# Optimization experiments

Measured on AMD Instinct MI355X. Metric: run time of the kernel, lower is better.

Reference implementation:

```python
import jax, jax.numpy as jnp
import numpy as np

NUM_HEADS = 16


def setup_inputs() -> dict:
    key = jax.random.key(0)
    ks = jax.random.split(key, 5)
    B, S, D = 2, 2048, 1024
    scale = 1.0 / np.sqrt(D)
    return {
        "hidden_states": jax.random.normal(ks[0], (B, S, D), dtype=jnp.float32),
        "Wq": jax.random.normal(ks[1], (D, D), dtype=jnp.float32) * scale,
        "bq": jnp.zeros((D,), jnp.float32),
        "Wk": jax.random.normal(ks[2], (D, D), dtype=jnp.float32) * scale,
        "bk": jnp.zeros((D,), jnp.float32),
        "Wv": jax.random.normal(ks[3], (D, D), dtype=jnp.float32) * scale,
        "bv": jnp.zeros((D,), jnp.float32),
        "Wo": jax.random.normal(ks[4], (D, D), dtype=jnp.float32) * scale,
        "bo": jnp.zeros((D,), jnp.float32),
    }


def reference(hidden_states, Wq, bq, Wk, bk, Wv, bv, Wo, bo):
    B, S, D = hidden_states.shape
    H = NUM_HEADS
    Dh = D // H

    def split_heads(x):  # [B,S,D] -> [B,H,S,Dh]
        return x.reshape(B, S, H, Dh).transpose(0, 2, 1, 3)

    q = split_heads(hidden_states @ Wq + bq)
    k = split_heads(hidden_states @ Wk + bk)
    v = split_heads(hidden_states @ Wv + bv)

    # causal additive mask: -inf strictly above the diagonal (triu, diagonal=1)
    i = jnp.arange(S)
    causal = jnp.where(i[None, :] > i[:, None], -jnp.inf, 0.0).astype(hidden_states.dtype)  # [S,S]

    scores = jnp.einsum("bhsd,bhtd->bhst", q, k) / jnp.sqrt(jnp.asarray(Dh, hidden_states.dtype))
    scores = scores + causal[None, None, :, :]
    weights = jax.nn.softmax(scores, axis=-1)  # [B,H,S,S]
    ctx = jnp.einsum("bhst,bhtd->bhsd", weights, v)
    ctx = ctx.transpose(0, 2, 1, 3).reshape(B, S, D)
    return ctx @ Wo + bo
```

## Files before the change

kernel.cpp:

```cpp
#include <hip/hip_runtime.h>
#include <math.h>

#define SEQ    2048
#define DMODEL 1024
#define NHEADS 16
#define DHEAD  64
#define NBATCH 2

typedef __attribute__((ext_vector_type(8)))  short bf16x8;
typedef __attribute__((ext_vector_type(4)))  float f32x4;
typedef __attribute__((ext_vector_type(16))) float f32x16;

__device__ __forceinline__ unsigned short f2bf(float f) {
    union { float f; unsigned u; } v; v.f = f;
    unsigned r = (v.u + 0x7FFF + ((v.u >> 16) & 1)) >> 16;
    return (unsigned short)r;
}

__device__ __forceinline__ unsigned cvt_pk_bf16(float lo, float hi) {
    unsigned r;
    asm("v_cvt_pk_bf16_f32 %0, %1, %2" : "=v"(r) : "v"(lo), "v"(hi));
    return r;
}

__device__ __forceinline__ void gload16(const void* g, void* l) {
    __builtin_amdgcn_global_load_lds(
        (const __attribute__((address_space(1))) unsigned*)g,
        (__attribute__((address_space(3))) unsigned*)l, 16, 0, 0);
}

__global__ __launch_bounds__(256)
void cast_bf16_kernel(const float* __restrict__ in, unsigned short* __restrict__ out) {
    const size_t g8 = ((size_t)blockIdx.x * 256 + threadIdx.x) * 8;
    float4 a = *reinterpret_cast<const float4*>(in + g8);
    float4 b = *reinterpret_cast<const float4*>(in + g8 + 4);
    bf16x8 o;
    o[0] = (short)f2bf(a.x); o[1] = (short)f2bf(a.y);
    o[2] = (short)f2bf(a.z); o[3] = (short)f2bf(a.w);
    o[4] = (short)f2bf(b.x); o[5] = (short)f2bf(b.y);
    o[6] = (short)f2bf(b.z); o[7] = (short)f2bf(b.w);
    *reinterpret_cast<bf16x8*>(out + g8) = o;
}

__global__ __launch_bounds__(256)
void wt_cast4_kernel(const float* __restrict__ W0, const float* __restrict__ W1,
                     const float* __restrict__ W2, const float* __restrict__ W3,
                     unsigned short* __restrict__ out) {
    __shared__ float tile[64][65];
    const int wsel = blockIdx.y;
    const float* W = (wsel == 0) ? W0 : (wsel == 1) ? W1 : (wsel == 2) ? W2 : W3;
    unsigned short* Wt = out + (size_t)wsel * 1024 * 1024;

    const int nt  = blockIdx.x & 15;
    const int kt  = blockIdx.x >> 4;
    const int tid = threadIdx.x;

#pragma unroll
    for (int r = 0; r < 4; ++r) {
        int kl = r * 16 + (tid >> 4);
        int nl = (tid & 15) * 4;
        float4 v = *reinterpret_cast<const float4*>(
            &W[(size_t)(kt * 64 + kl) * 1024 + nt * 64 + nl]);
        tile[kl][nl + 0] = v.x; tile[kl][nl + 1] = v.y;
        tile[kl][nl + 2] = v.z; tile[kl][nl + 3] = v.w;
    }
    __syncthreads();

    const int n  = tid >> 2;
    const int kc = (tid & 3) * 16;
    bf16x8 o0, o1;
#pragma unroll
    for (int i = 0; i < 8; ++i) o0[i] = (short)f2bf(tile[kc + i][n]);
#pragma unroll
    for (int i = 0; i < 8; ++i) o1[i] = (short)f2bf(tile[kc + 8 + i][n]);
    unsigned short* op = Wt + (size_t)(nt * 64 + n) * 1024 + kt * 64 + kc;
    *reinterpret_cast<bf16x8*>(op)     = o0;
    *reinterpret_cast<bf16x8*>(op + 8) = o1;
}

template <int MODE>
__global__ __launch_bounds__(256)
void gemm_bf16(const unsigned short* __restrict__ A,
               const unsigned short* __restrict__ Bt,
               const float* __restrict__ bias0, const float* __restrict__ bias1,
               const float* __restrict__ bias2,
               float* __restrict__ Cf,
               unsigned short* __restrict__ Qo, unsigned short* __restrict__ Ko,
               unsigned short* __restrict__ Vo,
               int M, int N, int K) {
    __shared__ unsigned short As[2][128 * 32];
    __shared__ unsigned short Bs[2][128 * 32];

    const int tid  = threadIdx.x;
    const int bm   = blockIdx.y * 128;
    const int bn   = blockIdx.x * 128;
    const int w    = tid >> 6;
    const int lane = tid & 63;
    const int lrow = lane & 15;
    const int lk   = lane >> 4;
    const int wm0  = (w >> 1) * 64;
    const int wn0  = (w & 1) * 64;

    const int boff0 = tid * 16;
    const int boff1 = 4096 + tid * 16;
    const int row0  = tid >> 2;
    const int row1  = 64 + row0;
    const int c     = tid & 3;
    const int sw0   = (c ^ ((row0 >> 1) & 3)) * 8;
    const int sw1   = (c ^ ((row1 >> 1) & 3)) * 8;

    const unsigned short* Ag = A  + (size_t)bm * K;
    const unsigned short* Bg = Bt + (size_t)bn * K;

    f32x4 acc[4][4];
#pragma unroll
    for (int i = 0; i < 4; ++i)
#pragma unroll
        for (int j = 0; j < 4; ++j) acc[i][j] = (f32x4){0.f, 0.f, 0.f, 0.f};

    const int NT = K / 32;
    {
        gload16(Ag + (size_t)row0 * K + sw0, (char*)&As[0][0] + boff0);
        gload16(Ag + (size_t)row1 * K + sw1, (char*)&As[0][0] + boff1);
        gload16(Bg + (size_t)row0 * K + sw0, (char*)&Bs[0][0] + boff0);
        gload16(Bg + (size_t)row1 * K + sw1, (char*)&Bs[0][0] + boff1);
    }
    __syncthreads();

    int buf = 0;
    for (int kt = 0; kt < NT; ++kt) {
        if (kt + 1 < NT) {
            const int k0 = (kt + 1) * 32;
            gload16(Ag + (size_t)row0 * K + k0 + sw0, (char*)&As[buf ^ 1][0] + boff0);
            gload16(Ag + (size_t)row1 * K + k0 + sw1, (char*)&As[buf ^ 1][0] + boff1);
            gload16(Bg + (size_t)row0 * K + k0 + sw0, (char*)&Bs[buf ^ 1][0] + boff0);
            gload16(Bg + (size_t)row1 * K + k0 + sw1, (char*)&Bs[buf ^ 1][0] + boff1);
        }

        bf16x8 af[4], bf[4];
#pragma unroll
        for (int mg = 0; mg < 4; ++mg) {
            const int r = wm0 + mg * 16 + lrow;
            af[mg] = *reinterpret_cast<const bf16x8*>(
                (char*)&As[buf][0] + r * 64 + ((lk ^ ((r >> 1) & 3)) * 16));
        }
#pragma unroll
        for (int ng = 0; ng < 4; ++ng) {
            const int r = wn0 + ng * 16 + lrow;
            bf[ng] = *reinterpret_cast<const bf16x8*>(
                (char*)&Bs[buf][0] + r * 64 + ((lk ^ ((r >> 1) & 3)) * 16));
        }
#pragma unroll
        for (int mg = 0; mg < 4; ++mg)
#pragma unroll
            for (int ng = 0; ng < 4; ++ng)
                acc[mg][ng] = __builtin_amdgcn_mfma_f32_16x16x32_bf16(
                    af[mg], bf[ng], acc[mg][ng], 0, 0, 0);

        __syncthreads();
        buf ^= 1;
    }

    if (MODE == 0) {
        const int type = bn >> 10;
        const int nloc = bn & 1023;
        const float* bias = (type == 0) ? bias0 : (type == 1) ? bias1 : bias2;
        const float QSCALE = 0.125f * 1.44269504088896f;
#pragma unroll
        for (int ng = 0; ng < 4; ++ng) {
            const int col = nloc + wn0 + ng * 16 + lrow;
            const float bv = bias[col];
            const int h = col >> 6, d = col & 63;
#pragma unroll
            for (int mg = 0; mg < 4; ++mg) {
#pragma unroll
                for (int j = 0; j < 4; ++j) {
                    const int row = bm + wm0 + mg * 16 + lk * 4 + j;
                    const int b = row >> 11, s = row & 2047;
                    const float val = acc[mg][ng][j] + bv;
                    if (type == 0)
                        Qo[((size_t)(b * 16 + h) * SEQ + s) * 64 + d] = f2bf(val * QSCALE);
                    else if (type == 1)
                        Ko[((size_t)(b * 16 + h) * SEQ + s) * 64 + d] = f2bf(val);
                    else
                        Vo[((size_t)(b * 16 + h) * 64 + d) * SEQ + s] = f2bf(val);
                }
            }
        }
    } else {
#pragma unroll
        for (int ng = 0; ng < 4; ++ng) {
            const int col = bn + wn0 + ng * 16 + lrow;
            const float bv = bias0[col];
#pragma unroll
            for (int mg = 0; mg < 4; ++mg) {
#pragma unroll
                for (int j = 0; j < 4; ++j) {
                    const int row = bm + wm0 + mg * 16 + lk * 4 + j;
                    Cf[(size_t)row * N + col] = acc[mg][ng][j] + bv;
                }
            }
        }
    }
}

__global__ __launch_bounds__(256)
void attn_mfma_kernel(const unsigned short* __restrict__ Qg,
                      const unsigned short* __restrict__ Kg,
                      const unsigned short* __restrict__ Vtg,
                      unsigned short* __restrict__ CTX) {
    __shared__ __align__(16) unsigned short Ks[2][64 * 64];
    __shared__ __align__(16) unsigned short Vt[2][64 * 64];

    const int bid = blockIdx.x;
    const int xcd = bid & 7;
    const int s   = bid >> 3;
    const int bh  = xcd * 4 + (s & 3);
    const int rb  = s >> 2;
    const int b  = bh >> 4;
    const int h  = bh & 15;
    const int r0 = rb * 128;
    const int tid  = threadIdx.x;
    const int w    = tid >> 6;
    const int lane = tid & 63;
    const int qcol = lane & 31;
    const int hlf  = lane >> 5;
    const int wr0  = r0 + w * 32;
    const int qrow = wr0 + qcol;

    const unsigned short* Kb = Kg + ((size_t)bh * SEQ) * DHEAD;
    const unsigned short* Vb = Vtg + ((size_t)bh * DHEAD) * SEQ;

    bf16x8 qf[4];
    {
        const unsigned short* qp = Qg + ((size_t)bh * SEQ + qrow) * DHEAD + hlf * 8;
#pragma unroll
        for (int ksub = 0; ksub < 4; ++ksub)
            qf[ksub] = *reinterpret_cast<const bf16x8*>(qp + ksub * 16);
    }

    f32x16 O0, O1;
#pragma unroll
    for (int r = 0; r < 16; ++r) { O0[r] = 0.f; O1[r] = 0.f; }
    float m = -1e30f, l = 0.f;

    const int srow = tid >> 2;
    const int c0   = (tid & 3) * 16;
    const int sb0  = srow * 128 + ((c0 * 2) ^ ((srow & 7) << 4));
    const int sb1  = srow * 128 + (((c0 + 8) * 2) ^ ((srow & 7) << 4));

    bf16x8 rk0, rk1, rv0, rv1;
    {
        const unsigned short* kp = Kb + (size_t)srow * DHEAD + c0;
        const unsigned short* vp = Vb + (size_t)srow * SEQ + c0;
        rk0 = *reinterpret_cast<const bf16x8*>(kp);
        rk1 = *reinterpret_cast<const bf16x8*>(kp + 8);
        rv0 = *reinterpret_cast<const bf16x8*>(vp);
        rv1 = *reinterpret_cast<const bf16x8*>(vp + 8);
    }

    const int ntile = (r0 + 128) / 64;
    for (int t = 0; t < ntile; ++t) {
        const int j0 = t * 64;
        const int buf = t & 1;
        *reinterpret_cast<bf16x8*>((char*)&Ks[buf][0] + sb0) = rk0;
        *reinterpret_cast<bf16x8*>((char*)&Ks[buf][0] + sb1) = rk1;
        *reinterpret_cast<bf16x8*>((char*)&Vt[buf][0] + sb0) = rv0;
        *reinterpret_cast<bf16x8*>((char*)&Vt[buf][0] + sb1) = rv1;
        __syncthreads();
        if (t + 1 < ntile) {
            const int j1 = j0 + 64;
            const unsigned short* kp = Kb + (size_t)(j1 + srow) * DHEAD + c0;
            const unsigned short* vp = Vb + (size_t)srow * SEQ + j1 + c0;
            rk0 = *reinterpret_cast<const bf16x8*>(kp);
            rk1 = *reinterpret_cast<const bf16x8*>(kp + 8);
            rv0 = *reinterpret_cast<const bf16x8*>(vp);
            rv1 = *reinterpret_cast<const bf16x8*>(vp + 8);
        }

        if (j0 <= wr0 + 31) {
            f32x16 S[2];
#pragma unroll
            for (int r = 0; r < 16; ++r) { S[0][r] = 0.f; S[1][r] = 0.f; }
            __builtin_amdgcn_s_setprio(1);
#pragma unroll
            for (int kb = 0; kb < 2; ++kb) {
                const int key = kb * 32 + qcol;
#pragma unroll
                for (int ksub = 0; ksub < 4; ++ksub) {
                    int boff = key * 128 + ((ksub * 32 + hlf * 16) ^ ((key & 7) << 4));
                    bf16x8 kf = *reinterpret_cast<const bf16x8*>((char*)&Ks[buf][0] + boff);
                    S[kb] = __builtin_amdgcn_mfma_f32_32x32x16_bf16(
                        kf, qf[ksub], S[kb], 0, 0, 0);
                }
            }
            __builtin_amdgcn_s_setprio(0);

            if (j0 + 63 > wr0) {
#pragma unroll
                for (int kb = 0; kb < 2; ++kb)
#pragma unroll
                    for (int r = 0; r < 16; ++r) {
                        int ka = j0 + kb * 32 + (r & 3) + 8 * (r >> 2) + 4 * hlf;
                        if (ka > qrow) S[kb][r] = -1e30f;
                    }
            }

            float mx[8];
#pragma unroll
            for (int r = 0; r < 8; ++r)
                mx[r] = fmaxf(fmaxf(S[0][r], S[0][r + 8]),
                              fmaxf(S[1][r], S[1][r + 8]));
            float m01 = fmaxf(mx[0], mx[1]), m23 = fmaxf(mx[2], mx[3]);
            float m45 = fmaxf(mx[4], mx[5]), m67 = fmaxf(mx[6], mx[7]);
            float pm = fmaxf(fmaxf(m01, m23), fmaxf(m45, m67));
            pm = fmaxf(pm, __shfl_xor(pm, 32));

            if (__any(pm > m)) {
                float mnew = fmaxf(m, pm);
                float cor  = __builtin_amdgcn_exp2f(m - mnew);
                m = mnew;
                l *= cor;
#pragma unroll
                for (int r = 0; r < 16; ++r) { O0[r] *= cor; O1[r] *= cor; }
            }

            float l0 = 0.f, l1 = 0.f, l2 = 0.f, l3 = 0.f;
#pragma unroll
            for (int kb = 0; kb < 2; ++kb)
#pragma unroll
                for (int r = 0; r < 16; r += 4) {
                    float p0 = __builtin_amdgcn_exp2f(S[kb][r + 0] - m);
                    float p1 = __builtin_amdgcn_exp2f(S[kb][r + 1] - m);
                    float p2 = __builtin_amdgcn_exp2f(S[kb][r + 2] - m);
                    float p3 = __builtin_amdgcn_exp2f(S[kb][r + 3] - m);
                    S[kb][r + 0] = p0; S[kb][r + 1] = p1;
                    S[kb][r + 2] = p2; S[kb][r + 3] = p3;
                    l0 += p0; l1 += p1; l2 += p2; l3 += p3;
                }
            l += (l0 + l1) + (l2 + l3);

#pragma unroll
            for (int kc = 0; kc < 4; ++kc) {
                const int kb = kc >> 1;
                const int R0 = (kc & 1) * 8;
                unsigned pa = cvt_pk_bf16(S[kb][R0 + 0], S[kb][R0 + 1]);
                unsigned pc = cvt_pk_bf16(S[kb][R0 + 4], S[kb][R0 + 5]);
                asm("v_permlane32_swap_b32 %0, %1" : "+v"(pa), "+v"(pc));
                unsigned pb = cvt_pk_bf16(S[kb][R0 + 2], S[kb][R0 + 3]);
                unsigned pd = cvt_pk_bf16(S[kb][R0 + 6], S[kb][R0 + 7]);
                asm("v_permlane32_swap_b32 %0, %1" : "+v"(pb), "+v"(pd));
                union { unsigned u[4]; bf16x8 v; } pf;
                pf.u[0] = pa; pf.u[1] = pb; pf.u[2] = pc; pf.u[3] = pd;
                __builtin_amdgcn_s_setprio(1);
#pragma unroll
                for (int db = 0; db < 2; ++db) {
                    const int dim = db * 32 + qcol;
                    int boff = dim * 128 + ((kc * 32 + hlf * 16) ^ ((dim & 7) << 4));
                    bf16x8 vf = *reinterpret_cast<const bf16x8*>((char*)&Vt[buf][0] + boff);
                    if (db == 0)
                        O0 = __builtin_amdgcn_mfma_f32_32x32x16_bf16(vf, pf.v, O0, 0, 0, 0);
                    else
                        O1 = __builtin_amdgcn_mfma_f32_32x32x16_bf16(vf, pf.v, O1, 0, 0, 0);
                }
                __builtin_amdgcn_s_setprio(0);
            }
        }
    }

    l += __shfl_xor(l, 32);
    const float inv = 1.f / l;
    unsigned short* crow = CTX + ((size_t)(b * SEQ + qrow)) * DMODEL + h * DHEAD;
#pragma unroll
    for (int pq = 0; pq < 4; ++pq) {
        unsigned w0 = cvt_pk_bf16(O0[pq * 4 + 0] * inv, O0[pq * 4 + 1] * inv);
        unsigned w1 = cvt_pk_bf16(O0[pq * 4 + 2] * inv, O0[pq * 4 + 3] * inv);
        uint2 val; val.x = w0; val.y = w1;
        *reinterpret_cast<uint2*>(crow + 8 * pq + 4 * hlf) = val;
    }
#pragma unroll
    for (int pq = 0; pq < 4; ++pq) {
        unsigned w0 = cvt_pk_bf16(O1[pq * 4 + 0] * inv, O1[pq * 4 + 1] * inv);
        unsigned w1 = cvt_pk_bf16(O1[pq * 4 + 2] * inv, O1[pq * 4 + 3] * inv);
        uint2 val; val.x = w0; val.y = w1;
        *reinterpret_cast<uint2*>(crow + 32 + 8 * pq + 4 * hlf) = val;
    }
}

extern "C" void kernel_launch(void* const* d_in, const int* in_sizes, int n_in,
                              void* d_out, int out_size, void* d_ws, size_t ws_size,
                              hipStream_t stream) {
    const float* hs = (const float*)d_in[0];
    const float* Wq = (const float*)d_in[1];
    const float* bq = (const float*)d_in[2];
    const float* Wk = (const float*)d_in[3];
    const float* bk = (const float*)d_in[4];
    const float* Wv = (const float*)d_in[5];
    const float* bv = (const float*)d_in[6];
    const float* Wo = (const float*)d_in[7];
    const float* bo = (const float*)d_in[8];
    float* out = (float*)d_out;

    const size_t NTOK = (size_t)NBATCH * SEQ;
    unsigned short* hs_bf  = (unsigned short*)d_ws;
    unsigned short* Wqkv_t = hs_bf + NTOK * DMODEL;
    unsigned short* Wo_t   = Wqkv_t + 3072 * 1024;
    unsigned short* Qh     = Wo_t + 1024 * 1024;
    unsigned short* Kh     = Qh + NTOK * DMODEL;
    unsigned short* Vt     = Kh + NTOK * DMODEL;
    unsigned short* Cb     = Vt + NTOK * DMODEL;

    cast_bf16_kernel<<<(int)(NTOK * DMODEL / 8 / 256), 256, 0, stream>>>(hs, hs_bf);
    wt_cast4_kernel<<<dim3(256, 4), 256, 0, stream>>>(Wq, Wk, Wv, Wo, Wqkv_t);

    dim3 gqkv(3072 / 128, NTOK / 128);
    gemm_bf16<0><<<gqkv, 256, 0, stream>>>(hs_bf, Wqkv_t, bq, bk, bv,
                                           nullptr, Qh, Kh, Vt,
                                           (int)NTOK, 3072, DMODEL);

    attn_mfma_kernel<<<NBATCH * NHEADS * (SEQ / 128), 256, 0, stream>>>(Qh, Kh, Vt, Cb);

    dim3 go(DMODEL / 128, NTOK / 128);
    gemm_bf16<1><<<go, 256, 0, stream>>>(Cb, Wo_t, bo, nullptr, nullptr,
                                         out, nullptr, nullptr, nullptr,
                                         (int)NTOK, DMODEL, DMODEL);
}
```

Baseline: 134.8 us.

## Split attention key range across two warp groups with LDS merge

Each attention block now runs 512 threads: four warps per half handle alternating 64-key tiles of a 128-key chunk, so each query row's key range is split between two wave groups. The partial softmax states are merged through shared memory at the end. The block order is also remapped so causal row-blocks of differing length interleave. This aims to cut per-wave serial work and balance causal load, at the cost of larger LDS use, an extra merge step with barriers, and idle waves on diagonal tiles.

```diff
diff --git a/kernel.cpp b/kernel.cpp
--- a/kernel.cpp
+++ b/kernel.cpp
@@ -119,12 +119,10 @@
         for (int j = 0; j < 4; ++j) acc[i][j] = (f32x4){0.f, 0.f, 0.f, 0.f};
 
     const int NT = K / 32;
-    {
-        gload16(Ag + (size_t)row0 * K + sw0, (char*)&As[0][0] + boff0);
-        gload16(Ag + (size_t)row1 * K + sw1, (char*)&As[0][0] + boff1);
-        gload16(Bg + (size_t)row0 * K + sw0, (char*)&Bs[0][0] + boff0);
-        gload16(Bg + (size_t)row1 * K + sw1, (char*)&Bs[0][0] + boff1);
-    }
+    gload16(Ag + (size_t)row0 * K + sw0, (char*)&As[0][0] + boff0);
+    gload16(Ag + (size_t)row1 * K + sw1, (char*)&As[0][0] + boff1);
+    gload16(Bg + (size_t)row0 * K + sw0, (char*)&Bs[0][0] + boff0);
+    gload16(Bg + (size_t)row1 * K + sw1, (char*)&Bs[0][0] + boff1);
     __syncthreads();
 
     int buf = 0;
@@ -204,28 +202,30 @@
     }
 }
 
-__global__ __launch_bounds__(256)
+__global__ __launch_bounds__(512, 4)
 void attn_mfma_kernel(const unsigned short* __restrict__ Qg,
                       const unsigned short* __restrict__ Kg,
                       const unsigned short* __restrict__ Vtg,
                       unsigned short* __restrict__ CTX) {
-    __shared__ __align__(16) unsigned short Ks[2][64 * 64];
-    __shared__ __align__(16) unsigned short Vt[2][64 * 64];
+    __shared__ __align__(16) char smem[65536];
 
     const int bid = blockIdx.x;
     const int xcd = bid & 7;
     const int s   = bid >> 3;
     const int bh  = xcd * 4 + (s & 3);
-    const int rb  = s >> 2;
+    const int k   = s >> 2;
+    const int rb  = (k < 8) ? k : (23 - k);
     const int b  = bh >> 4;
     const int h  = bh & 15;
     const int r0 = rb * 128;
     const int tid  = threadIdx.x;
     const int w    = tid >> 6;
+    const int wrow = w & 3;
+    const int wkey = w >> 2;
     const int lane = tid & 63;
     const int qcol = lane & 31;
     const int hlf  = lane >> 5;
-    const int wr0  = r0 + w * 32;
+    const int wr0  = r0 + wrow * 32;
     const int qrow = wr0 + qcol;
 
     const unsigned short* Kb = Kg + ((size_t)bh * SEQ) * DHEAD;
@@ -244,41 +244,42 @@
     for (int r = 0; r < 16; ++r) { O0[r] = 0.f; O1[r] = 0.f; }
     float m = -1e30f, l = 0.f;
 
-    const int srow = tid >> 2;
-    const int c0   = (tid & 3) * 16;
-    const int sb0  = srow * 128 + ((c0 * 2) ^ ((srow & 7) << 4));
-    const int sb1  = srow * 128 + (((c0 + 8) * 2) ^ ((srow & 7) << 4));
+    const int srow  = tid >> 3;
+    const int slot  = tid & 7;
+    const int swz   = (slot * 16) ^ ((srow & 7) << 4);
+    const int dK0   = srow * 128 + swz;
+    const int dK1   = 8192 + srow * 128 + swz;
+    const int dV0   = 16384 + srow * 128 + swz;
+    const int dV1   = 24576 + srow * 128 + swz;
 
     bf16x8 rk0, rk1, rv0, rv1;
     {
-        const unsigned short* kp = Kb + (size_t)srow * DHEAD + c0;
-        const unsigned short* vp = Vb + (size_t)srow * SEQ + c0;
-        rk0 = *reinterpret_cast<const bf16x8*>(kp);
-        rk1 = *reinterpret_cast<const bf16x8*>(kp + 8);
-        rv0 = *reinterpret_cast<const bf16x8*>(vp);
-        rv1 = *reinterpret_cast<const bf16x8*>(vp + 8);
-    }
-
-    const int ntile = (r0 + 128) / 64;
-    for (int t = 0; t < ntile; ++t) {
-        const int j0 = t * 64;
-        const int buf = t & 1;
-        *reinterpret_cast<bf16x8*>((char*)&Ks[buf][0] + sb0) = rk0;
-        *reinterpret_cast<bf16x8*>((char*)&Ks[buf][0] + sb1) = rk1;
-        *reinterpret_cast<bf16x8*>((char*)&Vt[buf][0] + sb0) = rv0;
-        *reinterpret_cast<bf16x8*>((char*)&Vt[buf][0] + sb1) = rv1;
+        rk0 = *reinterpret_cast<const bf16x8*>(Kb + (size_t)srow * DHEAD + slot * 8);
+        rk1 = *reinterpret_cast<const bf16x8*>(Kb + (size_t)(64 + srow) * DHEAD + slot * 8);
+        rv0 = *reinterpret_cast<const bf16x8*>(Vb + (size_t)srow * SEQ + slot * 8);
+        rv1 = *reinterpret_cast<const bf16x8*>(Vb + (size_t)srow * SEQ + 64 + slot * 8);
+    }
+
+    const int nit = rb + 1;
+    for (int it = 0; it < nit; ++it) {
+        const int jc  = it * 128;
+        const int buf = (it & 1) * 32768;
+        *reinterpret_cast<bf16x8*>(smem + buf + dK0) = rk0;
+        *reinterpret_cast<bf16x8*>(smem + buf + dK1) = rk1;
+        *reinterpret_cast<bf16x8*>(smem + buf + dV0) = rv0;
+        *reinterpret_cast<bf16x8*>(smem + buf + dV1) = rv1;
         __syncthreads();
-        if (t + 1 < ntile) {
-            const int j1 = j0 + 64;
-            const unsigned short* kp = Kb + (size_t)(j1 + srow) * DHEAD + c0;
-            const unsigned short* vp = Vb + (size_t)srow * SEQ + j1 + c0;
-            rk0 = *reinterpret_cast<const bf16x8*>(kp);
-            rk1 = *reinterpret_cast<const bf16x8*>(kp + 8);
-            rv0 = *reinterpret_cast<const bf16x8*>(vp);
-            rv1 = *reinterpret_cast<const bf16x8*>(vp + 8);
-        }
-
+        if (it + 1 < nit) {
+            const int j1 = jc + 128;
+            rk0 = *reinterpret_cast<const bf16x8*>(Kb + (size_t)(j1 + srow) * DHEAD + slot * 8);
+            rk1 = *reinterpret_cast<const bf16x8*>(Kb + (size_t)(j1 + 64 + srow) * DHEAD + slot * 8);
+            rv0 = *reinterpret_cast<const bf16x8*>(Vb + (size_t)srow * SEQ + j1 + slot * 8);
+            rv1 = *reinterpret_cast<const bf16x8*>(Vb + (size_t)srow * SEQ + j1 + 64 + slot * 8);
+        }
+
+        const int j0 = jc + wkey * 64;
         if (j0 <= wr0 + 31) {
+            const int tb = buf + wkey * 8192;
             f32x16 S[2];
 #pragma unroll
             for (int r = 0; r < 16; ++r) { S[0][r] = 0.f; S[1][r] = 0.f; }
@@ -288,8 +289,8 @@
                 const int key = kb * 32 + qcol;
 #pragma unroll
                 for (int ksub = 0; ksub < 4; ++ksub) {
-                    int boff = key * 128 + ((ksub * 32 + hlf * 16) ^ ((key & 7) << 4));
-                    bf16x8 kf = *reinterpret_cast<const bf16x8*>((char*)&Ks[buf][0] + boff);
+                    int boff = tb + key * 128 + ((ksub * 32 + hlf * 16) ^ ((key & 7) << 4));
+                    bf16x8 kf = *reinterpret_cast<const bf16x8*>(smem + boff);
                     S[kb] = __builtin_amdgcn_mfma_f32_32x32x16_bf16(
                         kf, qf[ksub], S[kb], 0, 0, 0);
                 }
@@ -340,6 +341,7 @@
                 }
             l += (l0 + l1) + (l2 + l3);
 
+            const int vb2 = buf + 16384 + wkey * 8192;
 #pragma unroll
             for (int kc = 0; kc < 4; ++kc) {
                 const int kb = kc >> 1;
@@ -356,8 +358,8 @@
 #pragma unroll
                 for (int db = 0; db < 2; ++db) {
                     const int dim = db * 32 + qcol;
-                    int boff = dim * 128 + ((kc * 32 + hlf * 16) ^ ((dim & 7) << 4));
-                    bf16x8 vf = *reinterpret_cast<const bf16x8*>((char*)&Vt[buf][0] + boff);
+                    int boff = vb2 + dim * 128 + ((kc * 32 + hlf * 16) ^ ((dim & 7) << 4));
+                    bf16x8 vf = *reinterpret_cast<const bf16x8*>(smem + boff);
                     if (db == 0)
                         O0 = __builtin_amdgcn_mfma_f32_32x32x16_bf16(vf, pf.v, O0, 0, 0, 0);
                     else
@@ -368,22 +370,46 @@
         }
     }
 
-    l += __shfl_xor(l, 32);
-    const float inv = 1.f / l;
-    unsigned short* crow = CTX + ((size_t)(b * SEQ + qrow)) * DMODEL + h * DHEAD;
-#pragma unroll
-    for (int pq = 0; pq < 4; ++pq) {
-        unsigned w0 = cvt_pk_bf16(O0[pq * 4 + 0] * inv, O0[pq * 4 + 1] * inv);
-        unsigned w1 = cvt_pk_bf16(O0[pq * 4 + 2] * inv, O0[pq * 4 + 3] * inv);
-        uint2 val; val.x = w0; val.y = w1;
-        *reinterpret_cast<uint2*>(crow + 8 * pq + 4 * hlf) = val;
-    }
-#pragma unroll
-    for (int pq = 0; pq < 4; ++pq) {
-        unsigned w0 = cvt_pk_bf16(O1[pq * 4 + 0] * inv, O1[pq * 4 + 1] * inv);
-        unsigned w1 = cvt_pk_bf16(O1[pq * 4 + 2] * inv, O1[pq * 4 + 3] * inv);
-        uint2 val; val.x = w0; val.y = w1;
-        *reinterpret_cast<uint2*>(crow + 32 + 8 * pq + 4 * hlf) = val;
+    __syncthreads();
+    float* mb = (float*)smem;
+    if (wkey == 1) {
+        float* dst = mb + ((size_t)(wrow * 64 + lane)) * 36;
+        dst[0] = m; dst[1] = l;
+#pragma unroll
+        for (int r = 0; r < 16; ++r) dst[2 + r]  = O0[r];
+#pragma unroll
+        for (int r = 0; r < 16; ++r) dst[18 + r] = O1[r];
+    }
+    __syncthreads();
+    if (wkey == 0) {
+        const float* src = mb + ((size_t)(wrow * 64 + lane)) * 36;
+        float mB = src[0], lB = src[1];
+        float mf = fmaxf(m, mB);
+        float sA = __builtin_amdgcn_exp2f(m - mf);
+        float sB = __builtin_amdgcn_exp2f(mB - mf);
+        l = l * sA + lB * sB;
+#pragma unroll
+        for (int r = 0; r < 16; ++r) O0[r] = O0[r] * sA + src[2 + r]  * sB;
+#pragma unroll
+        for (int r = 0; r < 16; ++r) O1[r] = O1[r] * sA + src[18 + r] * sB;
+
+        l += __shfl_xor(l, 32);
+        const float inv = 1.f / l;
+        unsigned short* crow = CTX + ((size_t)(b * SEQ + qrow)) * DMODEL + h * DHEAD;
+#pragma unroll
+        for (int pq = 0; pq < 4; ++pq) {
+            unsigned w0 = cvt_pk_bf16(O0[pq * 4 + 0] * inv, O0[pq * 4 + 1] * inv);
+            unsigned w1 = cvt_pk_bf16(O0[pq * 4 + 2] * inv, O0[pq * 4 + 3] * inv);
+            uint2 val; val.x = w0; val.y = w1;
+            *reinterpret_cast<uint2*>(crow + 8 * pq + 4 * hlf) = val;
+        }
+#pragma unroll
+        for (int pq = 0; pq < 4; ++pq) {
+            unsigned w0 = cvt_pk_bf16(O1[pq * 4 + 0] * inv, O1[pq * 4 + 1] * inv);
+            unsigned w1 = cvt_pk_bf16(O1[pq * 4 + 2] * inv, O1[pq * 4 + 3] * inv);
+            uint2 val; val.x = w0; val.y = w1;
+            *reinterpret_cast<uint2*>(crow + 32 + 8 * pq + 4 * hlf) = val;
+        }
     }
 }
 
@@ -418,7 +444,7 @@
                                            nullptr, Qh, Kh, Vt,
                                            (int)NTOK, 3072, DMODEL);
 
-    attn_mfma_kernel<<<NBATCH * NHEADS * (SEQ / 128), 256, 0, stream>>>(Qh, Kh, Vt, Cb);
+    attn_mfma_kernel<<<512, 512, 0, stream>>>(Qh, Kh, Vt, Cb);
 
     dim3 go(DMODEL / 128, NTOK / 128);
     gemm_bf16<1><<<go, 256, 0, stream>>>(Cb, Wo_t, bo, nullptr, nullptr,
```

After: 133.6 us. About the same (-0.9%).

## Add 256x256 eight-phase pipelined QKV GEMM and balance causal attention block order

Applied to the files above, without the earlier changes.

Replaces the 128x128 QKV projection GEMM with a 256x256 tile kernel using 512 threads, 128KB LDS double buffering, XOR-swizzled layout and quadrant-phased loads interleaved with MFMA under raised priority. Attention blocks now pair early and late causal row blocks in launch order to balance work. The larger tile raises reuse but launches only 192 blocks, which may underfill the GPU; the GEMM is also specialised to K=1024.

```diff
diff --git a/kernel.cpp b/kernel.cpp
--- a/kernel.cpp
+++ b/kernel.cpp
@@ -28,6 +28,10 @@
         (const __attribute__((address_space(1))) unsigned*)g,
         (__attribute__((address_space(3))) unsigned*)l, 16, 0, 0);
 }
+
+#define VW(n)  asm volatile("s_waitcnt vmcnt(" #n ")" ::: "memory")
+#define BAR()  do { asm volatile("" ::: "memory"); __builtin_amdgcn_s_barrier(); \
+                    asm volatile("" ::: "memory"); } while (0)
 
 __global__ __launch_bounds__(256)
 void cast_bf16_kernel(const float* __restrict__ in, unsigned short* __restrict__ out) {
@@ -78,15 +82,174 @@
     *reinterpret_cast<bf16x8*>(op + 8) = o1;
 }
 
+__device__ __forceinline__ void q8_lda(const char* smem, int buf, int mh,
+                                       int wr, int lrow, int lk, bf16x8 af[4][2]) {
+#pragma unroll
+    for (int mf4 = 0; mf4 < 4; ++mf4) {
+        const int row = mh * 128 + wr * 64 + mf4 * 16 + lrow;
+#pragma unroll
+        for (int ks = 0; ks < 2; ++ks) {
+            const int ch = (ks * 4 + lk) ^ (row & 7);
+            af[mf4][ks] = *reinterpret_cast<const bf16x8*>(
+                smem + buf * 65536 + row * 128 + ch * 16);
+        }
+    }
+}
+__device__ __forceinline__ void q8_ldb(const char* smem, int buf, int nh,
+                                       int wc, int lrow, int lk, bf16x8 bf[2][2]) {
+#pragma unroll
+    for (int nf2 = 0; nf2 < 2; ++nf2) {
+        const int row = nh * 128 + wc * 32 + nf2 * 16 + lrow;
+#pragma unroll
+        for (int ks = 0; ks < 2; ++ks) {
+            const int ch = (ks * 4 + lk) ^ (row & 7);
+            bf[nf2][ks] = *reinterpret_cast<const bf16x8*>(
+                smem + buf * 65536 + 32768 + row * 128 + ch * 16);
+        }
+    }
+}
+__device__ __forceinline__ void q8_stage(char* smem, int buf, int op, int half,
+                                         int kt, int tid, int rl0, int ch0,
+                                         const unsigned short* Ag,
+                                         const unsigned short* Bg) {
+    const unsigned short* G = op ? Bg : Ag;
+    char* lb = smem + buf * 65536 + op * 32768 + half * 16384;
+    gload16(G + (size_t)(half * 128 + rl0) * 1024 + kt * 64 + ch0 * 8,
+            lb + tid * 16);
+    gload16(G + (size_t)(half * 128 + rl0 + 64) * 1024 + kt * 64 + ch0 * 8,
+            lb + 8192 + tid * 16);
+}
+#define Q8_MM(mh, nh)                                                         \
+    do {                                                                      \
+        __builtin_amdgcn_s_setprio(1);                                        \
+        _Pragma("unroll")                                                     \
+        for (int mf4 = 0; mf4 < 4; ++mf4)                                     \
+            _Pragma("unroll")                                                 \
+            for (int nf2 = 0; nf2 < 2; ++nf2)                                 \
+                _Pragma("unroll")                                             \
+                for (int ks = 0; ks < 2; ++ks)                                \
+                    acc[(mh)*4 + mf4][(nh)*2 + nf2] =                         \
+                        __builtin_amdgcn_mfma_f32_16x16x32_bf16(              \
+                            af[mf4][ks], bf[nf2][ks],                         \
+                            acc[(mh)*4 + mf4][(nh)*2 + nf2], 0, 0, 0);        \
+        __builtin_amdgcn_s_setprio(0);                                        \
+    } while (0)
+
+template <int DOSTAGE>
+__device__ __forceinline__ void q8_halfiter(char* smem, int buf, int sbuf, int skt,
+                                            int tid, int wr, int wc, int lrow,
+                                            int lk, int rl0, int ch0,
+                                            const unsigned short* Ag,
+                                            const unsigned short* Bg,
+                                            f32x4 (&acc)[8][4]) {
+    bf16x8 af[4][2], bf[2][2];
+    VW(4); BAR();
+    q8_lda(smem, buf, 0, wr, lrow, lk, af);
+    q8_ldb(smem, buf, 0, wc, lrow, lk, bf);
+    if (DOSTAGE) q8_stage(smem, sbuf, 0, 0, skt, tid, rl0, ch0, Ag, Bg);
+    BAR();
+    Q8_MM(0, 0);
+    if (DOSTAGE) { VW(4); } else { VW(2); }
+    BAR();
+    q8_ldb(smem, buf, 1, wc, lrow, lk, bf);
+    if (DOSTAGE) q8_stage(smem, sbuf, 1, 0, skt, tid, rl0, ch0, Ag, Bg);
+    BAR();
+    Q8_MM(0, 1);
+    if (DOSTAGE) { VW(4); } else { VW(0); }
+    BAR();
+    q8_lda(smem, buf, 1, wr, lrow, lk, af);
+    q8_ldb(smem, buf, 0, wc, lrow, lk, bf);
+    if (DOSTAGE) q8_stage(smem, sbuf, 1, 1, skt, tid, rl0, ch0, Ag, Bg);
+    BAR();
+    Q8_MM(1, 0);
+    BAR();
+    q8_ldb(smem, buf, 1, wc, lrow, lk, bf);
+    if (DOSTAGE) q8_stage(smem, sbuf, 0, 1, skt, tid, rl0, ch0, Ag, Bg);
+    BAR();
+    Q8_MM(1, 1);
+}
+
+__global__ __launch_bounds__(512, 2)
+void gemm_qkv_8ph(const unsigned short* __restrict__ A,
+                  const unsigned short* __restrict__ Bt,
+                  const float* __restrict__ bq, const float* __restrict__ bk,
+                  const float* __restrict__ bv,
+                  unsigned short* __restrict__ Qo, unsigned short* __restrict__ Ko,
+                  unsigned short* __restrict__ Vo) {
+    extern __shared__ char smem[];
+    const int tid  = threadIdx.x;
+    const int wid  = tid >> 6;
+    const int lane = tid & 63;
+    const int wr   = wid >> 2;
+    const int wc   = wid & 3;
+    const int lrow = lane & 15;
+    const int lk   = lane >> 4;
+    const int bm   = blockIdx.y * 256;
+    const int bn   = blockIdx.x * 256;
+    const int rl0  = tid >> 3;
+    const int ch0  = (tid & 7) ^ (rl0 & 7);
+
+    const unsigned short* Ag = A  + (size_t)bm * 1024;
+    const unsigned short* Bg = Bt + (size_t)bn * 1024;
+
+    f32x4 acc[8][4];
+#pragma unroll
+    for (int i = 0; i < 8; ++i)
+#pragma unroll
+        for (int j = 0; j < 4; ++j) acc[i][j] = (f32x4){0.f, 0.f, 0.f, 0.f};
+
+    q8_stage(smem, 0, 0, 0, 0, tid, rl0, ch0, Ag, Bg);
+    q8_stage(smem, 0, 1, 0, 0, tid, rl0, ch0, Ag, Bg);
+    q8_stage(smem, 0, 1, 1, 0, tid, rl0, ch0, Ag, Bg);
+    q8_stage(smem, 0, 0, 1, 0, tid, rl0, ch0, Ag, Bg);
+
+    for (int j = 0; j < 8; ++j) {
+        q8_halfiter<1>(smem, 0, 1, 2 * j + 1, tid, wr, wc, lrow, lk, rl0, ch0,
+                       Ag, Bg, acc);
+        if (j < 7)
+            q8_halfiter<1>(smem, 1, 0, 2 * j + 2, tid, wr, wc, lrow, lk, rl0, ch0,
+                           Ag, Bg, acc);
+        else
+            q8_halfiter<0>(smem, 1, 0, 0, tid, wr, wc, lrow, lk, rl0, ch0,
+                           Ag, Bg, acc);
+    }
+
+    const float QSCALE = 0.125f * 1.44269504088896f;
+#pragma unroll
+    for (int nf = 0; nf < 4; ++nf) {
+        const int col  = bn + ((nf < 2) ? (wc * 32 + nf * 16)
+                                        : (128 + wc * 32 + (nf - 2) * 16)) + lrow;
+        const int type = col >> 10;
+        const int colq = col & 1023;
+        const float bvv = ((type == 0) ? bq : (type == 1) ? bk : bv)[colq];
+        const int h = colq >> 6, d = colq & 63;
+#pragma unroll
+        for (int mf = 0; mf < 8; ++mf) {
+            const int rbase = bm + ((mf < 4) ? (wr * 64 + mf * 16)
+                                             : (128 + wr * 64 + (mf - 4) * 16))
+                              + lk * 4;
+#pragma unroll
+            for (int jj = 0; jj < 4; ++jj) {
+                const int row = rbase + jj;
+                const int b = row >> 11, s = row & 2047;
+                const float val = acc[mf][nf][jj] + bvv;
+                if (type == 0)
+                    Qo[((size_t)(b * 16 + h) * SEQ + s) * 64 + d] = f2bf(val * QSCALE);
+                else if (type == 1)
+                    Ko[((size_t)(b * 16 + h) * SEQ + s) * 64 + d] = f2bf(val);
+                else
+                    Vo[((size_t)(b * 16 + h) * 64 + d) * SEQ + s] = f2bf(val);
+            }
+        }
+    }
+}
+
 template <int MODE>
 __global__ __launch_bounds__(256)
 void gemm_bf16(const unsigned short* __restrict__ A,
                const unsigned short* __restrict__ Bt,
-               const float* __restrict__ bias0, const float* __restrict__ bias1,
-               const float* __restrict__ bias2,
+               const float* __restrict__ bias0,
                float* __restrict__ Cf,
-               unsigned short* __restrict__ Qo, unsigned short* __restrict__ Ko,
-               unsigned short* __restrict__ Vo,
                int M, int N, int K) {
     __shared__ unsigned short As[2][128 * 32];
     __shared__ unsigned short Bs[2][128 * 32];
@@ -119,12 +282,10 @@
         for (int j = 0; j < 4; ++j) acc[i][j] = (f32x4){0.f, 0.f, 0.f, 0.f};
 
     const int NT = K / 32;
-    {
-        gload16(Ag + (size_t)row0 * K + sw0, (char*)&As[0][0] + boff0);
-        gload16(Ag + (size_t)row1 * K + sw1, (char*)&As[0][0] + boff1);
-        gload16(Bg + (size_t)row0 * K + sw0, (char*)&Bs[0][0] + boff0);
-        gload16(Bg + (size_t)row1 * K + sw1, (char*)&Bs[0][0] + boff1);
-    }
+    gload16(Ag + (size_t)row0 * K + sw0, (char*)&As[0][0] + boff0);
+    gload16(Ag + (size_t)row1 * K + sw1, (char*)&As[0][0] + boff1);
+    gload16(Bg + (size_t)row0 * K + sw0, (char*)&Bs[0][0] + boff0);
+    gload16(Bg + (size_t)row1 * K + sw1, (char*)&Bs[0][0] + boff1);
     __syncthreads();
 
     int buf = 0;
@@ -161,44 +322,16 @@
         buf ^= 1;
     }
 
-    if (MODE == 0) {
-        const int type = bn >> 10;
-        const int nloc = bn & 1023;
-        const float* bias = (type == 0) ? bias0 : (type == 1) ? bias1 : bias2;
-        const float QSCALE = 0.125f * 1.44269504088896f;
-#pragma unroll
-        for (int ng = 0; ng < 4; ++ng) {
-            const int col = nloc + wn0 + ng * 16 + lrow;
-            const float bv = bias[col];
-            const int h = col >> 6, d = col & 63;
-#pragma unroll
-            for (int mg = 0; mg < 4; ++mg) {
-#pragma unroll
-                for (int j = 0; j < 4; ++j) {
-                    const int row = bm + wm0 + mg * 16 + lk * 4 + j;
-                    const int b = row >> 11, s = row & 2047;
-                    const float val = acc[mg][ng][j] + bv;
-                    if (type == 0)
-                        Qo[((size_t)(b * 16 + h) * SEQ + s) * 64 + d] = f2bf(val * QSCALE);
-                    else if (type == 1)
-                        Ko[((size_t)(b * 16 + h) * SEQ + s) * 64 + d] = f2bf(val);
-                    else
-                        Vo[((size_t)(b * 16 + h) * 64 + d) * SEQ + s] = f2bf(val);
-                }
-            }
-        }
-    } else {
-#pragma unroll
-        for (int ng = 0; ng < 4; ++ng) {
-            const int col = bn + wn0 + ng * 16 + lrow;
-            const float bv = bias0[col];
-#pragma unroll
-            for (int mg = 0; mg < 4; ++mg) {
-#pragma unroll
-                for (int j = 0; j < 4; ++j) {
-                    const int row = bm + wm0 + mg * 16 + lk * 4 + j;
-                    Cf[(size_t)row * N + col] = acc[mg][ng][j] + bv;
-                }
+#pragma unroll
+    for (int ng = 0; ng < 4; ++ng) {
+        const int col = bn + wn0 + ng * 16 + lrow;
+        const float bvv = bias0[col];
+#pragma unroll
+        for (int mg = 0; mg < 4; ++mg) {
+#pragma unroll
+            for (int j = 0; j < 4; ++j) {
+                const int row = bm + wm0 + mg * 16 + lk * 4 + j;
+                Cf[(size_t)row * N + col] = acc[mg][ng][j] + bvv;
             }
         }
     }
@@ -216,7 +349,8 @@
     const int xcd = bid & 7;
     const int s   = bid >> 3;
     const int bh  = xcd * 4 + (s & 3);
-    const int rb  = s >> 2;
+    const int k2  = s >> 2;
+    const int rb  = (k2 < 8) ? k2 : (23 - k2);
     const int b  = bh >> 4;
     const int h  = bh & 15;
     const int r0 = rb * 128;
@@ -413,15 +547,13 @@
     cast_bf16_kernel<<<(int)(NTOK * DMODEL / 8 / 256), 256, 0, stream>>>(hs, hs_bf);
     wt_cast4_kernel<<<dim3(256, 4), 256, 0, stream>>>(Wq, Wk, Wv, Wo, Wqkv_t);
 
-    dim3 gqkv(3072 / 128, NTOK / 128);
-    gemm_bf16<0><<<gqkv, 256, 0, stream>>>(hs_bf, Wqkv_t, bq, bk, bv,
-                                           nullptr, Qh, Kh, Vt,
-                                           (int)NTOK, 3072, DMODEL);
+    dim3 gqkv(3072 / 256, (int)NTOK / 256);
+    gemm_qkv_8ph<<<gqkv, 512, 131072, stream>>>(hs_bf, Wqkv_t, bq, bk, bv,
+                                                Qh, Kh, Vt);
 
     attn_mfma_kernel<<<NBATCH * NHEADS * (SEQ / 128), 256, 0, stream>>>(Qh, Kh, Vt, Cb);
 
-    dim3 go(DMODEL / 128, NTOK / 128);
-    gemm_bf16<1><<<go, 256, 0, stream>>>(Cb, Wo_t, bo, nullptr, nullptr,
-                                         out, nullptr, nullptr, nullptr,
+    dim3 go(DMODEL / 128, (int)NTOK / 128);
+    gemm_bf16<1><<<go, 256, 0, stream>>>(Cb, Wo_t, bo, out,
                                          (int)NTOK, DMODEL, DMODEL);
 }
```

Measured after the change: 273.4 us. 2.03x slower.

## Add XCD-aware GEMM tile swizzle, separate V transpose kernel, balance causal row blocks

Applied to the files above, without the earlier changes.

The GEMMs now use a 1D grid remapped so that tiles sharing A/B panels land on the same XCD, which is meant to improve L2 reuse. The QKV epilogue no longer does strided transposed writes for V. It writes V row-major, and a new small kernel transposes it through shared memory into the layout attention expects. The attention kernel's row-block order is changed to pair heavy and light causal blocks for better load balance. In exchange this adds an extra launch, extra workspace and one more pass over V.

```diff
diff --git a/kernel.cpp b/kernel.cpp
--- a/kernel.cpp
+++ b/kernel.cpp
@@ -76,6 +76,32 @@
     unsigned short* op = Wt + (size_t)(nt * 64 + n) * 1024 + kt * 64 + kc;
     *reinterpret_cast<bf16x8*>(op)     = o0;
     *reinterpret_cast<bf16x8*>(op + 8) = o1;
+}
+
+__global__ __launch_bounds__(256)
+void vt_kernel(const unsigned short* __restrict__ Vh, unsigned short* __restrict__ Vt) {
+    __shared__ unsigned short tile[64][72];
+    const int bid = blockIdx.x;
+    const int st  = bid & 31;
+    const int bh  = bid >> 5;
+    const int s0  = st * 64;
+    const int tid = threadIdx.x;
+
+    const int sl = tid >> 2;
+    const int dc = (tid & 3) * 16;
+    const unsigned short* src = Vh + ((size_t)bh * SEQ + s0 + sl) * 64 + dc;
+    *reinterpret_cast<bf16x8*>(&tile[sl][dc])     = *reinterpret_cast<const bf16x8*>(src);
+    *reinterpret_cast<bf16x8*>(&tile[sl][dc + 8]) = *reinterpret_cast<const bf16x8*>(src + 8);
+    __syncthreads();
+
+    const int dl = tid >> 2;
+    const int sc = (tid & 3) * 16;
+    unsigned short tmp[16];
+#pragma unroll
+    for (int k2 = 0; k2 < 16; ++k2) tmp[k2] = tile[sc + k2][dl];
+    unsigned short* dst = Vt + ((size_t)bh * 64 + dl) * SEQ + s0 + sc;
+    *reinterpret_cast<bf16x8*>(dst)     = *reinterpret_cast<bf16x8*>(&tmp[0]);
+    *reinterpret_cast<bf16x8*>(dst + 8) = *reinterpret_cast<bf16x8*>(&tmp[8]);
 }
 
 template <int MODE>
@@ -91,9 +117,20 @@
     __shared__ unsigned short As[2][128 * 32];
     __shared__ unsigned short Bs[2][128 * 32];
 
+    int bx, by;
+    {
+        const int xcd = blockIdx.x & 7, i = blockIdx.x >> 3;
+        if (MODE == 0) {
+            bx = (xcd >> 2) * 12 + i % 12;
+            by = (xcd & 3) * 8 + i / 12;
+        } else {
+            bx = (xcd & 1) * 4 + i % 4;
+            by = (xcd >> 1) * 8 + i / 4;
+        }
+    }
     const int tid  = threadIdx.x;
-    const int bm   = blockIdx.y * 128;
-    const int bn   = blockIdx.x * 128;
+    const int bm   = by * 128;
+    const int bn   = bx * 128;
     const int w    = tid >> 6;
     const int lane = tid & 63;
     const int lrow = lane & 15;
@@ -119,12 +156,10 @@
         for (int j = 0; j < 4; ++j) acc[i][j] = (f32x4){0.f, 0.f, 0.f, 0.f};
 
     const int NT = K / 32;
-    {
-        gload16(Ag + (size_t)row0 * K + sw0, (char*)&As[0][0] + boff0);
-        gload16(Ag + (size_t)row1 * K + sw1, (char*)&As[0][0] + boff1);
-        gload16(Bg + (size_t)row0 * K + sw0, (char*)&Bs[0][0] + boff0);
-        gload16(Bg + (size_t)row1 * K + sw1, (char*)&Bs[0][0] + boff1);
-    }
+    gload16(Ag + (size_t)row0 * K + sw0, (char*)&As[0][0] + boff0);
+    gload16(Ag + (size_t)row1 * K + sw1, (char*)&As[0][0] + boff1);
+    gload16(Bg + (size_t)row0 * K + sw0, (char*)&Bs[0][0] + boff0);
+    gload16(Bg + (size_t)row1 * K + sw1, (char*)&Bs[0][0] + boff1);
     __syncthreads();
 
     int buf = 0;
@@ -165,7 +200,8 @@
         const int type = bn >> 10;
         const int nloc = bn & 1023;
         const float* bias = (type == 0) ? bias0 : (type == 1) ? bias1 : bias2;
-        const float QSCALE = 0.125f * 1.44269504088896f;
+        unsigned short* dst = (type == 0) ? Qo : (type == 1) ? Ko : Vo;
+        const float scale = (type == 0) ? (0.125f * 1.44269504088896f) : 1.0f;
 #pragma unroll
         for (int ng = 0; ng < 4; ++ng) {
             const int col = nloc + wn0 + ng * 16 + lrow;
@@ -177,13 +213,8 @@
                 for (int j = 0; j < 4; ++j) {
                     const int row = bm + wm0 + mg * 16 + lk * 4 + j;
                     const int b = row >> 11, s = row & 2047;
-                    const float val = acc[mg][ng][j] + bv;
-                    if (type == 0)
-                        Qo[((size_t)(b * 16 + h) * SEQ + s) * 64 + d] = f2bf(val * QSCALE);
-                    else if (type == 1)
-                        Ko[((size_t)(b * 16 + h) * SEQ + s) * 64 + d] = f2bf(val);
-                    else
-                        Vo[((size_t)(b * 16 + h) * 64 + d) * SEQ + s] = f2bf(val);
+                    const float val = (acc[mg][ng][j] + bv) * scale;
+                    dst[((size_t)(b * 16 + h) * SEQ + s) * 64 + d] = f2bf(val);
                 }
             }
         }
@@ -216,7 +247,8 @@
     const int xcd = bid & 7;
     const int s   = bid >> 3;
     const int bh  = xcd * 4 + (s & 3);
-    const int rb  = s >> 2;
+    const int k2  = s >> 2;
+    const int rb  = (k2 < 8) ? k2 : (23 - k2);
     const int b  = bh >> 4;
     const int h  = bh & 15;
     const int r0 = rb * 128;
@@ -407,21 +439,22 @@
     unsigned short* Wo_t   = Wqkv_t + 3072 * 1024;
     unsigned short* Qh     = Wo_t + 1024 * 1024;
     unsigned short* Kh     = Qh + NTOK * DMODEL;
-    unsigned short* Vt     = Kh + NTOK * DMODEL;
+    unsigned short* Vh     = Kh + NTOK * DMODEL;
+    unsigned short* Vt     = Vh + NTOK * DMODEL;
     unsigned short* Cb     = Vt + NTOK * DMODEL;
 
     cast_bf16_kernel<<<(int)(NTOK * DMODEL / 8 / 256), 256, 0, stream>>>(hs, hs_bf);
     wt_cast4_kernel<<<dim3(256, 4), 256, 0, stream>>>(Wq, Wk, Wv, Wo, Wqkv_t);
 
-    dim3 gqkv(3072 / 128, NTOK / 128);
-    gemm_bf16<0><<<gqkv, 256, 0, stream>>>(hs_bf, Wqkv_t, bq, bk, bv,
-                                           nullptr, Qh, Kh, Vt,
-                                           (int)NTOK, 3072, DMODEL);
+    gemm_bf16<0><<<768, 256, 0, stream>>>(hs_bf, Wqkv_t, bq, bk, bv,
+                                          nullptr, Qh, Kh, Vh,
+                                          (int)NTOK, 3072, DMODEL);
+
+    vt_kernel<<<1024, 256, 0, stream>>>(Vh, Vt);
 
     attn_mfma_kernel<<<NBATCH * NHEADS * (SEQ / 128), 256, 0, stream>>>(Qh, Kh, Vt, Cb);
 
-    dim3 go(DMODEL / 128, NTOK / 128);
-    gemm_bf16<1><<<go, 256, 0, stream>>>(Cb, Wo_t, bo, nullptr, nullptr,
-                                         out, nullptr, nullptr, nullptr,
-                                         (int)NTOK, DMODEL, DMODEL);
-}
+    gemm_bf16<1><<<256, 256, 0, stream>>>(Cb, Wo_t, bo, nullptr, nullptr,
+                                          out, nullptr, nullptr, nullptr,
+                                          (int)NTOK, DMODEL, DMODEL);
+}
```

New measurement: 125.3 us. 1.08x faster.
